# Performance work log

Hardware: AMD Instinct MI355X
Metric: run time of the kernel (lower is better)

## Reference

```python
import jax, jax.numpy as jnp
import numpy as np

C = 512
GROUPS = 32
EPS = 1e-5


def group_norm(x, gamma, beta):
    # x: (B, C, H, W)
    B, Ch, H, W = x.shape
    xg = x.reshape(B, GROUPS, Ch // GROUPS, H, W)
    mu = xg.mean(axis=(2, 3, 4), keepdims=True)
    var = xg.var(axis=(2, 3, 4), keepdims=True)
    xn = ((xg - mu) * jax.lax.rsqrt(var + EPS)).reshape(B, Ch, H, W)
    return xn * gamma[None, :, None, None] + beta[None, :, None, None]


def conv1x1(x, w, b):
    # 1x1 conv == per-pixel matmul; x: (B,C,H,W), w: (Cout,Cin), b: (Cout,)
    return jnp.einsum('bchw,oc->bohw', x, w) + b[None, :, None, None]


def setup_inputs() -> dict:
    key = jax.random.key(0)
    ks = jax.random.split(key, 12)
    B, H, W = 4, 64, 64
    s = 1.0 / np.sqrt(C)
    inp = {
        'x': jax.random.normal(ks[0], (B, C, H, W), dtype=jnp.float32),
        'gn_w': jnp.ones((C,), dtype=jnp.float32),
        'gn_b': jnp.zeros((C,), dtype=jnp.float32),
        'wq': jax.random.uniform(ks[1], (C, C), jnp.float32, -s, s),
        'bq': jax.random.uniform(ks[2], (C,), jnp.float32, -s, s),
        'wk': jax.random.uniform(ks[3], (C, C), jnp.float32, -s, s),
        'bk': jax.random.uniform(ks[4], (C,), jnp.float32, -s, s),
        'wv': jax.random.uniform(ks[5], (C, C), jnp.float32, -s, s),
        'bv': jax.random.uniform(ks[6], (C,), jnp.float32, -s, s),
        'wo': jax.random.uniform(ks[7], (C, C), jnp.float32, -s, s),
        'bo': jax.random.uniform(ks[8], (C,), jnp.float32, -s, s),
    }
    return inp


def reference(x, gn_w, gn_b, wq, bq, wk, bk, wv, bv, wo, bo):
    B, Ch, H, W = x.shape
    h = group_norm(x, gn_w, gn_b)
    q = conv1x1(h, wq, bq).reshape(B, Ch, H * W)  # (B,C,HW)
    k = conv1x1(h, wk, bk).reshape(B, Ch, H * W)
    v = conv1x1(h, wv, bv).reshape(B, Ch, H * W)
    scale = 1.0 / jnp.sqrt(jnp.float32(Ch))
    # scores: (B, HW_q, HW_k)
    w = jnp.einsum('bcq,bck->bqk', q, k) * scale
    w = jax.nn.softmax(w, axis=-1)
    o = jnp.einsum('bqk,bck->bcq', w, v).reshape(B, Ch, H, W)
    o = conv1x1(o, wo, bo)
    return x + o
```

## Files before the change

### kernel.cpp

```cpp
#include <hip/hip_runtime.h>


typedef _Float16 f16;
typedef _Float16 f16x8 __attribute__((ext_vector_type(8)));
typedef float f32x4 __attribute__((ext_vector_type(4)));

__device__ __forceinline__ void load_lds16(const void* g, void* l) {
  __builtin_amdgcn_global_load_lds(
      (const __attribute__((address_space(1))) unsigned int*)g,
      (__attribute__((address_space(3))) unsigned int*)l, 16, 0, 0);
}

__device__ __forceinline__ f32x4 mfma16(f16x8 a, f16x8 b, f32x4 c) {
  return __builtin_amdgcn_mfma_f32_16x16x32_f16(a, b, c, 0, 0, 0);
}

__global__ __launch_bounds__(256) void prep_weights(
    const float* __restrict__ wq, const float* __restrict__ bq,
    const float* __restrict__ wk, const float* __restrict__ bk,
    const float* __restrict__ wv, const float* __restrict__ wo,
    f16* __restrict__ Wqk, float* __restrict__ bqk,
    f16* __restrict__ Wv, f16* __restrict__ Wo) {
  const float s = 0.04419417382415922f;
  int i = blockIdx.x * 256 + threadIdx.x;
  if (i < 524288) {
    int row = i >> 9;
    Wqk[i] = (f16)((row < 512) ? wq[i] * s : wk[i - 262144]);
  } else if (i < 786432) {
    Wv[i - 524288] = (f16)wv[i - 524288];
  } else if (i < 1048576) {
    Wo[i - 786432] = (f16)wo[i - 786432];
  }
  if (i < 1024) bqk[i] = (i < 512) ? bq[i] * s : bk[i - 512];
}

__global__ __launch_bounds__(256) void gn_stats(const float* __restrict__ x,
                                                float2* __restrict__ stats) {
  long base = (long)blockIdx.x * 65536;
  int tid = threadIdx.x;
  float s = 0.f, ss = 0.f;
  for (int i = tid; i < 16384; i += 256) {
    float4 v = *(const float4*)&x[base + (long)i * 4];
    s += v.x + v.y + v.z + v.w;
    ss += v.x * v.x + v.y * v.y + v.z * v.z + v.w * v.w;
  }
#pragma unroll
  for (int o = 32; o; o >>= 1) {
    s += __shfl_xor(s, o);
    ss += __shfl_xor(ss, o);
  }
  __shared__ float rs[4], rss[4];
  if ((tid & 63) == 0) { rs[tid >> 6] = s; rss[tid >> 6] = ss; }
  __syncthreads();
  if (tid == 0) {
    s = rs[0] + rs[1] + rs[2] + rs[3];
    ss = rss[0] + rss[1] + rss[2] + rss[3];
    float mean = s * (1.f / 65536.f);
    float var = ss * (1.f / 65536.f) - mean * mean;
    stats[blockIdx.x] = make_float2(mean, rsqrtf(var + 1e-5f));
  }
}

__global__ __launch_bounds__(256) void gn_apply(
    const float* __restrict__ x, const float2* __restrict__ stats,
    const float* __restrict__ gnw, const float* __restrict__ gnb,
    f16* __restrict__ h_t) {
  int b = blockIdx.x >> 6;
  int p0 = (blockIdx.x & 63) * 64;
  int tid = threadIdx.x;
  __shared__ __align__(16) f16 lds[64 * 520];
  int c0 = tid >> 4;
  int p4 = tid & 15;
  for (int it = 0; it < 32; ++it) {
    int c = it * 16 + c0;
    float2 st = stats[b * 32 + (c >> 4)];
    float a = st.y * gnw[c];
    float sh = gnb[c] - st.x * a;
    float4 v = *(const float4*)&x[((long)(b * 512 + c)) * 4096 + p0 + p4 * 4];
    int pr = p4 * 4;
    lds[(pr + 0) * 520 + c] = (f16)(v.x * a + sh);
    lds[(pr + 1) * 520 + c] = (f16)(v.y * a + sh);
    lds[(pr + 2) * 520 + c] = (f16)(v.z * a + sh);
    lds[(pr + 3) * 520 + c] = (f16)(v.w * a + sh);
  }
  __syncthreads();
  for (int it = 0; it < 16; ++it) {
    int cid = it * 256 + tid;
    int prow = cid >> 6, c8 = (cid & 63) * 8;
    *(f16x8*)&h_t[((long)(b * 4096 + p0 + prow)) * 512 + c8] =
        *(const f16x8*)&lds[prow * 520 + c8];
  }
}

template <int MODE>
__global__ __launch_bounds__(256) void gemm_bt(
    const f16* __restrict__ A, int lda, long sAz,
    const f16* __restrict__ B, int ldb, long sBz,
    void* __restrict__ C, int ldc, long sCz,
    const float* __restrict__ bias,
    const float* __restrict__ resid, long sRz,
    int M, int N, int K) {
  __shared__ __align__(16) f16 tA[4096];
  __shared__ __align__(16) f16 tB[4096];
  const f16* Az = A + (long)blockIdx.z * sAz;
  const f16* Bz = B + (long)blockIdx.z * sBz;
  int tid = threadIdx.x, lane = tid & 63, wid = tid >> 6;
  long bm = (long)blockIdx.x * 128, bn = (long)blockIdx.y * 128;
  int srow = lane >> 2, scol = (lane & 3) * 8;
  int wrow = (wid >> 1) * 64, wcol = (wid & 1) * 64;
  int r = lane & 15, kb = (lane >> 4) * 8;

  const f16* gA0 = Az + (bm + wid * 32 + srow) * (long)lda + scol;
  const f16* gA1 = gA0 + 16 * (long)lda;
  const f16* gB0 = Bz + (bn + wid * 32 + srow) * (long)ldb + scol;
  const f16* gB1 = gB0 + 16 * (long)ldb;
  f16* lA0 = &tA[wid * 1024];
  f16* lA1 = &tA[wid * 1024 + 512];
  f16* lB0 = &tB[wid * 1024];
  f16* lB1 = &tB[wid * 1024 + 512];

  f32x4 acc[4][4];
#pragma unroll
  for (int i = 0; i < 4; ++i)
#pragma unroll
    for (int j = 0; j < 4; ++j) acc[i][j] = (f32x4){0.f, 0.f, 0.f, 0.f};

  for (int kt = 0; kt < K; kt += 32) {
    load_lds16(gA0 + kt, lA0);
    load_lds16(gA1 + kt, lA1);
    load_lds16(gB0 + kt, lB0);
    load_lds16(gB1 + kt, lB1);
    __syncthreads();
    f16x8 af[4], bfr[4];
#pragma unroll
    for (int mf = 0; mf < 4; ++mf)
      af[mf] = *(const f16x8*)&tA[(wrow + mf * 16 + r) * 32 + kb];
#pragma unroll
    for (int nf = 0; nf < 4; ++nf)
      bfr[nf] = *(const f16x8*)&tB[(wcol + nf * 16 + r) * 32 + kb];
#pragma unroll
    for (int mf = 0; mf < 4; ++mf)
#pragma unroll
      for (int nf = 0; nf < 4; ++nf)
        acc[mf][nf] = mfma16(af[mf], bfr[nf], acc[mf][nf]);
    __syncthreads();
  }

  long zC = (long)blockIdx.z * sCz;
  int r0 = (lane >> 4) * 4, cc = lane & 15;
#pragma unroll
  for (int mf = 0; mf < 4; ++mf) {
#pragma unroll
    for (int rr = 0; rr < 4; ++rr) {
      long R = bm + wrow + mf * 16 + r0 + rr;
      float badd = 0.f;
      if constexpr (MODE == 1 || MODE == 3) badd = bias[R];
#pragma unroll
      for (int nf = 0; nf < 4; ++nf) {
        long gc = bn + wcol + nf * 16 + cc;
        float v = acc[mf][nf][rr];
        if constexpr (MODE == 0) v += bias[gc];
        if constexpr (MODE == 1) v += badd;
        if constexpr (MODE == 3)
          v += badd + resid[(long)blockIdx.z * sRz + R * (long)ldc + gc];
        long idx = zC + R * (long)ldc + gc;
        if constexpr (MODE == 3)
          ((float*)C)[idx] = v;
        else
          ((f16*)C)[idx] = (f16)v;
      }
    }
  }
}

__global__ __launch_bounds__(256) void attn_fused(
    const f16* __restrict__ qk_t, const f16* __restrict__ v_ws,
    f16* __restrict__ o_t) {
  __shared__ __align__(16) char SMEM[107776];
  f16* KL = (f16*)SMEM;
  float* SP = (float*)(SMEM + 65536);
  f16* PL = (f16*)(SMEM + 102400);
  float* LSUM = (float*)(SMEM + 107520);
  f16* OL = (f16*)SMEM;

  const int tid = threadIdx.x;
  const int lane = tid & 63, w = tid >> 6;
  const int lq = lane & 15, lg = lane >> 4;
  const int z = blockIdx.y;
  const long bm = (long)blockIdx.x * 64;
  const int dq = w * 128;
  const f16* Qb = qk_t + (long)z * 4096 * 1024;
  const f16* Kb = Qb + 512;
  const f16* Vb = v_ws + (long)z * 4096;

  f16x8 qf[4][4];
#pragma unroll
  for (int nq = 0; nq < 4; ++nq)
#pragma unroll
    for (int s = 0; s < 4; ++s)
      qf[nq][s] = *(const f16x8*)
          &Qb[(bm + nq * 16 + lq) * 1024 + dq + s * 32 + lg * 8];

  f32x4 acc[4][8];
#pragma unroll
  for (int i = 0; i < 4; ++i)
#pragma unroll
    for (int j = 0; j < 8; ++j) acc[i][j] = (f32x4){0.f, 0.f, 0.f, 0.f};
  float rs = 0.f;

  auto stageK = [&](int kt, int b) {
#pragma unroll
    for (int i = 0; i < 8; ++i) {
      int rrow = w * 8 + i;
      const f16* src = &Kb[((long)(kt * 32 + rrow)) * 1024 +
                           ((lane * 8) ^ ((rrow & 7) << 3))];
      f16* dst = &KL[b * 16384 + rrow * 512];
      load_lds16(src, dst);
    }
  };

  stageK(0, 0);
  __syncthreads();

  for (int kt = 0; kt < 128; ++kt) {
    const int cur = kt & 1;
    f16x8 vf[8];
#pragma unroll
    for (int nf = 0; nf < 8; ++nf)
      vf[nf] = *(const f16x8*)
          &Vb[(long)(dq + nf * 16 + lq) * 16384 + kt * 32 + lg * 8];
    if (kt + 1 < 128) stageK(kt + 1, cur ^ 1);

    f32x4 sa[2][4];
#pragma unroll
    for (int i = 0; i < 2; ++i)
#pragma unroll
      for (int j = 0; j < 4; ++j) sa[i][j] = (f32x4){0.f, 0.f, 0.f, 0.f};
#pragma unroll
    for (int s = 0; s < 4; ++s) {
      f16x8 kf[2];
#pragma unroll
      for (int mf = 0; mf < 2; ++mf) {
        int row = mf * 16 + lq;
        int col = (dq + s * 32 + lg * 8) ^ ((row & 7) << 3);
        kf[mf] = *(const f16x8*)&KL[cur * 16384 + row * 512 + col];
      }
#pragma unroll
      for (int mf = 0; mf < 2; ++mf)
#pragma unroll
        for (int nq = 0; nq < 4; ++nq)
          sa[mf][nq] = mfma16(kf[mf], qf[nq][s], sa[mf][nq]);
    }
#pragma unroll
    for (int mf = 0; mf < 2; ++mf)
#pragma unroll
      for (int nq = 0; nq < 4; ++nq)
        *(f32x4*)&SP[(w * 64 + nq * 16 + lq) * 36 + mf * 16 + lg * 4] =
            sa[mf][nq];

    asm volatile("s_waitcnt lgkmcnt(0)" ::: "memory");
    __builtin_amdgcn_sched_barrier(0);
    __builtin_amdgcn_s_barrier();
    __builtin_amdgcn_sched_barrier(0);

    f32x4 u0 = (f32x4){0.f, 0.f, 0.f, 0.f};
    f32x4 u1 = (f32x4){0.f, 0.f, 0.f, 0.f};
#pragma unroll
    for (int pw = 0; pw < 4; ++pw) {
      int base = (pw * 64 + w * 16 + lq) * 36 + lg * 8;
      u0 += *(const f32x4*)&SP[base];
      u1 += *(const f32x4*)&SP[base + 4];
    }
    f16x8 pf;
    float psum = 0.f;
#pragma unroll
    for (int j = 0; j < 4; ++j) {
      float e0 = __expf(fminf(u0[j], 11.f));
      float e1 = __expf(fminf(u1[j], 11.f));
      pf[j] = (f16)e0;
      pf[4 + j] = (f16)e1;
      psum += e0 + e1;
    }
    rs += psum;
    *(f16x8*)&PL[(w * 16 + lq) * 40 + lg * 8] = pf;

    __syncthreads();

    f16x8 pa[4];
#pragma unroll
    for (int mf = 0; mf < 4; ++mf)
      pa[mf] = *(const f16x8*)&PL[(mf * 16 + lq) * 40 + lg * 8];
#pragma unroll
    for (int mf = 0; mf < 4; ++mf)
#pragma unroll
      for (int nf = 0; nf < 8; ++nf)
        acc[mf][nf] = mfma16(pa[mf], vf[nf], acc[mf][nf]);
  }

  rs += __shfl_xor(rs, 16);
  rs += __shfl_xor(rs, 32);
  if (lane < 16) LSUM[w * 16 + lane] = rs;
  __syncthreads();

  float li[4][4];
#pragma unroll
  for (int mf = 0; mf < 4; ++mf)
#pragma unroll
    for (int rr = 0; rr < 4; ++rr)
      li[mf][rr] = 1.f / LSUM[mf * 16 + lg * 4 + rr];

#pragma unroll
  for (int mf = 0; mf < 4; ++mf)
#pragma unroll
    for (int nf = 0; nf < 8; ++nf)
#pragma unroll
      for (int rr = 0; rr < 4; ++rr)
        OL[(mf * 16 + lg * 4 + rr) * 520 + dq + nf * 16 + lq] =
            (f16)(acc[mf][nf][rr] * li[mf][rr]);
  __syncthreads();

  f16* orow = o_t + ((long)z * 4096 + bm) * 512;
#pragma unroll
  for (int it = 0; it < 16; ++it) {
    int idx = it * 256 + tid;
    int row = idx >> 6, ch = (idx & 63) * 8;
    *(f16x8*)&orow[(long)row * 512 + ch] = *(const f16x8*)&OL[row * 520 + ch];
  }
}

extern "C" void kernel_launch(void* const* d_in, const int* in_sizes, int n_in,
                              void* d_out, int out_size, void* d_ws,
                              size_t ws_size, hipStream_t stream) {
  (void)in_sizes; (void)n_in; (void)out_size; (void)ws_size;
  const float* x   = (const float*)d_in[0];
  const float* gnw = (const float*)d_in[1];
  const float* gnb = (const float*)d_in[2];
  const float* wq  = (const float*)d_in[3];
  const float* bq  = (const float*)d_in[4];
  const float* wk  = (const float*)d_in[5];
  const float* bk  = (const float*)d_in[6];
  const float* wv  = (const float*)d_in[7];
  const float* bv  = (const float*)d_in[8];
  const float* wo  = (const float*)d_in[9];
  const float* bo  = (const float*)d_in[10];
  float* out = (float*)d_out;

  char* p = (char*)d_ws;
  auto alloc = [&](size_t bytes) {
    char* r = p;
    p += (bytes + 255) & ~(size_t)255;
    return r;
  };
  f16* Wqk    = (f16*)alloc(1024 * 512 * 2);
  float* bqk  = (float*)alloc(1024 * 4);
  f16* Wv     = (f16*)alloc(512 * 512 * 2);
  f16* Wo     = (f16*)alloc(512 * 512 * 2);
  float2* st  = (float2*)alloc(128 * 8);
  f16* h_t    = (f16*)alloc(16384L * 512 * 2);
  f16* qk_t   = (f16*)alloc(16384L * 1024 * 2);
  f16* v_ws   = (f16*)alloc(512L * 16384 * 2);
  f16* o_t    = (f16*)alloc(16384L * 512 * 2);

  prep_weights<<<4096, 256, 0, stream>>>(wq, bq, wk, bk, wv, wo, Wqk, bqk, Wv,
                                         Wo);
  gn_stats<<<128, 256, 0, stream>>>(x, st);
  gn_apply<<<256, 256, 0, stream>>>(x, st, gnw, gnb, h_t);

  gemm_bt<0><<<dim3(128, 8, 1), 256, 0, stream>>>(
      h_t, 512, 0, Wqk, 512, 0, qk_t, 1024, 0, bqk, nullptr, 0,
      16384, 1024, 512);
  gemm_bt<1><<<dim3(4, 128, 1), 256, 0, stream>>>(
      Wv, 512, 0, h_t, 512, 0, v_ws, 16384, 0, bv, nullptr, 0,
      512, 16384, 512);

  attn_fused<<<dim3(64, 4), 256, 0, stream>>>(qk_t, v_ws, o_t);

  gemm_bt<3><<<dim3(4, 32, 4), 256, 0, stream>>>(
      Wo, 512, 0, o_t, 512, 4096L * 512, out, 4096, 512L * 4096,
      bo, x, 512L * 4096, 512, 4096, 512);
}
```

Baseline: 462.8 us.

## Repartition attention so each wave owns query rows, staging V through LDS

The attention kernel now assigns each wave 16 full query rows across all 512 channels, in place of splitting the head dimension across waves. This removes the cross-wave score reduction through shared memory and the P tile exchange, so exp and the PV MFMAs run directly from registers using 16x16x16 MFMAs. V tiles are now double-buffered in LDS with async global-to-LDS loads alongside K, and block indices are remapped to interleave batches. The change raises register pressure (32 accumulators plus 16 Q fragments per lane) and uses the full 128KB of LDS, limiting occupancy to one block per CU.

Measured after the change: 604.1 us. +30.5%, slower.

```diff
diff --git a/kernel.cpp b/kernel.cpp
--- a/kernel.cpp
+++ b/kernel.cpp
@@ -3,6 +3,7 @@
 
 typedef _Float16 f16;
 typedef _Float16 f16x8 __attribute__((ext_vector_type(8)));
+typedef _Float16 f16x4 __attribute__((ext_vector_type(4)));
 typedef float f32x4 __attribute__((ext_vector_type(4)));
 
 __device__ __forceinline__ void load_lds16(const void* g, void* l) {
@@ -13,6 +14,9 @@
 
 __device__ __forceinline__ f32x4 mfma16(f16x8 a, f16x8 b, f32x4 c) {
   return __builtin_amdgcn_mfma_f32_16x16x32_f16(a, b, c, 0, 0, 0);
+}
+__device__ __forceinline__ f32x4 mfma16k16(f16x4 a, f16x4 b, f32x4 c) {
+  return __builtin_amdgcn_mfma_f32_16x16x16f16(a, b, c, 0, 0, 0);
 }
 
 __global__ __launch_bounds__(256) void prep_weights(
@@ -173,158 +177,135 @@
   }
 }
 
-__global__ __launch_bounds__(256) void attn_fused(
+__global__ __launch_bounds__(256, 1) void attn_fused2(
     const f16* __restrict__ qk_t, const f16* __restrict__ v_ws,
     f16* __restrict__ o_t) {
-  __shared__ __align__(16) char SMEM[107776];
+  __shared__ __align__(16) char SMEM[131072];
   f16* KL = (f16*)SMEM;
-  float* SP = (float*)(SMEM + 65536);
-  f16* PL = (f16*)(SMEM + 102400);
-  float* LSUM = (float*)(SMEM + 107520);
+  f16* VL = (f16*)(SMEM + 65536);
   f16* OL = (f16*)SMEM;
 
   const int tid = threadIdx.x;
   const int lane = tid & 63, w = tid >> 6;
   const int lq = lane & 15, lg = lane >> 4;
-  const int z = blockIdx.y;
-  const long bm = (long)blockIdx.x * 64;
-  const int dq = w * 128;
+  const int bid = blockIdx.x;
+  const int z = (bid >> 1) & 3;
+  const int qblk = ((bid >> 3) << 1) | (bid & 1);
+  const long bm = (long)qblk * 64;
   const f16* Qb = qk_t + (long)z * 4096 * 1024;
   const f16* Kb = Qb + 512;
   const f16* Vb = v_ws + (long)z * 4096;
 
-  f16x8 qf[4][4];
-#pragma unroll
-  for (int nq = 0; nq < 4; ++nq)
-#pragma unroll
-    for (int s = 0; s < 4; ++s)
-      qf[nq][s] = *(const f16x8*)
-          &Qb[(bm + nq * 16 + lq) * 1024 + dq + s * 32 + lg * 8];
-
-  f32x4 acc[4][8];
-#pragma unroll
-  for (int i = 0; i < 4; ++i)
-#pragma unroll
-    for (int j = 0; j < 8; ++j) acc[i][j] = (f32x4){0.f, 0.f, 0.f, 0.f};
+  f16x8 qf[16];
+#pragma unroll
+  for (int s = 0; s < 16; ++s)
+    qf[s] = *(const f16x8*)&Qb[(bm + w * 16 + lq) * 1024 + s * 32 + lg * 8];
+
+  f32x4 acc[32];
+#pragma unroll
+  for (int i = 0; i < 32; ++i) acc[i] = (f32x4){0.f, 0.f, 0.f, 0.f};
   float rs = 0.f;
-
-  auto stageK = [&](int kt, int b) {
-#pragma unroll
-    for (int i = 0; i < 8; ++i) {
-      int rrow = w * 8 + i;
-      const f16* src = &Kb[((long)(kt * 32 + rrow)) * 1024 +
-                           ((lane * 8) ^ ((rrow & 7) << 3))];
-      f16* dst = &KL[b * 16384 + rrow * 512];
-      load_lds16(src, dst);
-    }
-  };
-
-  stageK(0, 0);
-  __syncthreads();
 
   for (int kt = 0; kt < 128; ++kt) {
     const int cur = kt & 1;
-    f16x8 vf[8];
-#pragma unroll
-    for (int nf = 0; nf < 8; ++nf)
-      vf[nf] = *(const f16x8*)
-          &Vb[(long)(dq + nf * 16 + lq) * 16384 + kt * 32 + lg * 8];
-    if (kt + 1 < 128) stageK(kt + 1, cur ^ 1);
-
-    f32x4 sa[2][4];
-#pragma unroll
-    for (int i = 0; i < 2; ++i)
-#pragma unroll
-      for (int j = 0; j < 4; ++j) sa[i][j] = (f32x4){0.f, 0.f, 0.f, 0.f};
-#pragma unroll
-    for (int s = 0; s < 4; ++s) {
-      f16x8 kf[2];
-#pragma unroll
-      for (int mf = 0; mf < 2; ++mf) {
-        int row = mf * 16 + lq;
-        int col = (dq + s * 32 + lg * 8) ^ ((row & 7) << 3);
-        kf[mf] = *(const f16x8*)&KL[cur * 16384 + row * 512 + col];
-      }
-#pragma unroll
-      for (int mf = 0; mf < 2; ++mf)
-#pragma unroll
-        for (int nq = 0; nq < 4; ++nq)
-          sa[mf][nq] = mfma16(kf[mf], qf[nq][s], sa[mf][nq]);
-    }
-#pragma unroll
-    for (int mf = 0; mf < 2; ++mf)
-#pragma unroll
-      for (int nq = 0; nq < 4; ++nq)
-        *(f32x4*)&SP[(w * 64 + nq * 16 + lq) * 36 + mf * 16 + lg * 4] =
-            sa[mf][nq];
-
-    asm volatile("s_waitcnt lgkmcnt(0)" ::: "memory");
-    __builtin_amdgcn_sched_barrier(0);
-    __builtin_amdgcn_s_barrier();
-    __builtin_amdgcn_sched_barrier(0);
-
-    f32x4 u0 = (f32x4){0.f, 0.f, 0.f, 0.f};
-    f32x4 u1 = (f32x4){0.f, 0.f, 0.f, 0.f};
-#pragma unroll
-    for (int pw = 0; pw < 4; ++pw) {
-      int base = (pw * 64 + w * 16 + lq) * 36 + lg * 8;
-      u0 += *(const f32x4*)&SP[base];
-      u1 += *(const f32x4*)&SP[base + 4];
-    }
-    f16x8 pf;
+    if (kt == 0) {
+#pragma unroll
+      for (int i = 0; i < 8; ++i) {
+        int row = w * 8 + i;
+        load_lds16(&Kb[((long)row) * 1024 + ((lane * 8) ^ ((row & 7) << 3))],
+                   &KL[row * 512]);
+      }
+#pragma unroll
+      for (int i = 0; i < 8; ++i) {
+        int chunk = w * 8 + i;
+        int d = chunk * 16 + (lane >> 2);
+        load_lds16(&Vb[(long)d * 16384 + (((lane & 3) * 8) ^ ((d & 3) << 3))],
+                   &VL[chunk * 512]);
+      }
+      __syncthreads();
+    }
+    if (kt + 1 < 128) {
+      const int nb = (cur ^ 1) * 16384;
+      const int kn = (kt + 1) * 32;
+#pragma unroll
+      for (int i = 0; i < 8; ++i) {
+        int row = w * 8 + i;
+        load_lds16(
+            &Kb[((long)(kn + row)) * 1024 + ((lane * 8) ^ ((row & 7) << 3))],
+            &KL[nb + row * 512]);
+      }
+#pragma unroll
+      for (int i = 0; i < 8; ++i) {
+        int chunk = w * 8 + i;
+        int d = chunk * 16 + (lane >> 2);
+        load_lds16(
+            &Vb[(long)d * 16384 + kn + (((lane & 3) * 8) ^ ((d & 3) << 3))],
+            &VL[nb + chunk * 512]);
+      }
+    }
+
+    f32x4 sa0 = (f32x4){0.f, 0.f, 0.f, 0.f};
+    f32x4 sa1 = (f32x4){0.f, 0.f, 0.f, 0.f};
+    const int kbase = cur * 16384;
+#pragma unroll
+    for (int s = 0; s < 16; ++s) {
+      int r0 = lq;
+      int r1 = 16 + lq;
+      f16x8 kf0 = *(const f16x8*)
+          &KL[kbase + r0 * 512 + ((s * 32 + lg * 8) ^ ((r0 & 7) << 3))];
+      f16x8 kf1 = *(const f16x8*)
+          &KL[kbase + r1 * 512 + ((s * 32 + lg * 8) ^ ((r1 & 7) << 3))];
+      sa0 = mfma16(kf0, qf[s], sa0);
+      sa1 = mfma16(kf1, qf[s], sa1);
+    }
+
+    f16x4 pa0, pa1;
     float psum = 0.f;
 #pragma unroll
-    for (int j = 0; j < 4; ++j) {
-      float e0 = __expf(fminf(u0[j], 11.f));
-      float e1 = __expf(fminf(u1[j], 11.f));
-      pf[j] = (f16)e0;
-      pf[4 + j] = (f16)e1;
+    for (int rr = 0; rr < 4; ++rr) {
+      float e0 = __expf(fminf(sa0[rr], 11.f));
+      float e1 = __expf(fminf(sa1[rr], 11.f));
       psum += e0 + e1;
+      pa0[rr] = (f16)e0;
+      pa1[rr] = (f16)e1;
     }
     rs += psum;
-    *(f16x8*)&PL[(w * 16 + lq) * 40 + lg * 8] = pf;
+
+    const int vbase = cur * 16384;
+#pragma unroll
+    for (int nf = 0; nf < 32; ++nf) {
+      int d = nf * 16 + lq;
+      int vrow = vbase + d * 32;
+      f16x4 vf0 = *(const f16x4*)&VL[vrow + ((lg * 4) ^ ((d & 3) << 3))];
+      f16x4 vf1 = *(const f16x4*)&VL[vrow + ((16 + lg * 4) ^ ((d & 3) << 3))];
+      acc[nf] = mfma16k16(pa0, vf0, acc[nf]);
+      acc[nf] = mfma16k16(pa1, vf1, acc[nf]);
+    }
 
     __syncthreads();
-
-    f16x8 pa[4];
-#pragma unroll
-    for (int mf = 0; mf < 4; ++mf)
-      pa[mf] = *(const f16x8*)&PL[(mf * 16 + lq) * 40 + lg * 8];
-#pragma unroll
-    for (int mf = 0; mf < 4; ++mf)
-#pragma unroll
-      for (int nf = 0; nf < 8; ++nf)
-        acc[mf][nf] = mfma16(pa[mf], vf[nf], acc[mf][nf]);
   }
 
   rs += __shfl_xor(rs, 16);
   rs += __shfl_xor(rs, 32);
-  if (lane < 16) LSUM[w * 16 + lane] = rs;
-  __syncthreads();
-
-  float li[4][4];
-#pragma unroll
-  for (int mf = 0; mf < 4; ++mf)
+  float linv = 1.f / rs;
+  float li[4];
+#pragma unroll
+  for (int rr = 0; rr < 4; ++rr) li[rr] = __shfl(linv, lg * 4 + rr);
+
+#pragma unroll
+  for (int nf = 0; nf < 32; ++nf)
 #pragma unroll
     for (int rr = 0; rr < 4; ++rr)
-      li[mf][rr] = 1.f / LSUM[mf * 16 + lg * 4 + rr];
-
-#pragma unroll
-  for (int mf = 0; mf < 4; ++mf)
-#pragma unroll
-    for (int nf = 0; nf < 8; ++nf)
-#pragma unroll
-      for (int rr = 0; rr < 4; ++rr)
-        OL[(mf * 16 + lg * 4 + rr) * 520 + dq + nf * 16 + lq] =
-            (f16)(acc[mf][nf][rr] * li[mf][rr]);
+      OL[(w * 16 + lg * 4 + rr) * 520 + nf * 16 + lq] =
+          (f16)(acc[nf][rr] * li[rr]);
   __syncthreads();
 
   f16* orow = o_t + ((long)z * 4096 + bm) * 512;
 #pragma unroll
   for (int it = 0; it < 16; ++it) {
     int idx = it * 256 + tid;
-    int row = idx >> 6, ch = (idx & 63) * 8;
-    *(f16x8*)&orow[(long)row * 512 + ch] = *(const f16x8*)&OL[row * 520 + ch];
+    int row = idx >> 6, c8 = (idx & 63) * 8;
+    *(f16x8*)&orow[(long)row * 512 + c8] = *(const f16x8*)&OL[row * 520 + c8];
   }
 }
 
@@ -373,7 +354,7 @@
       Wv, 512, 0, h_t, 512, 0, v_ws, 16384, 0, bv, nullptr, 0,
       512, 16384, 512);
 
-  attn_fused<<<dim3(64, 4), 256, 0, stream>>>(qk_t, v_ws, o_t);
+  attn_fused2<<<256, 256, 0, stream>>>(qk_t, v_ws, o_t);
 
   gemm_bt<3><<<dim3(4, 32, 4), 256, 0, stream>>>(
       Wo, 512, 0, o_t, 512, 4096L * 512, out, 4096, 512L * 4096,
```
